# Kernel optimization log

Hardware: AMD Instinct MI355X
Metric: run time of the kernel (lower is better)

Reference implementation:

```python
import jax, jax.numpy as jnp
import numpy as np
from jax import lax

C1, C2 = 64, 128
B, H2, W2 = 16, 64, 64
EPS = 1e-5


def conv2d(x, w, b, pad):
    y = lax.conv_general_dilated(x, w, (1, 1), [(pad, pad), (pad, pad)],
                                 dimension_numbers=('NCHW', 'OIHW', 'NCHW'))
    return y + b[None, :, None, None]


def batchnorm(x, g, be):
    # training-mode BN (batch statistics), matching torch nn.BatchNorm2d default
    m = jnp.mean(x, axis=(0, 2, 3), keepdims=True)
    v = jnp.var(x, axis=(0, 2, 3), keepdims=True)
    return (x - m) * jax.lax.rsqrt(v + EPS) * g[None, :, None, None] + be[None, :, None, None]


def up2_bilinear_ac(x):
    # bilinear upsample x2 with align_corners=True (nn.UpsamplingBilinear2d)
    b, c, h, w = x.shape
    yy = jnp.arange(2 * h, dtype=x.dtype) * ((h - 1) / (2 * h - 1))
    xx = jnp.arange(2 * w, dtype=x.dtype) * ((w - 1) / (2 * w - 1))
    y0 = jnp.floor(yy).astype(jnp.int32); y1 = jnp.minimum(y0 + 1, h - 1)
    x0 = jnp.floor(xx).astype(jnp.int32); x1 = jnp.minimum(x0 + 1, w - 1)
    wy = (yy - y0.astype(x.dtype))
    wx = (xx - x0.astype(x.dtype))
    rows = x[:, :, y0, :] * (1 - wy)[:, None] + x[:, :, y1, :] * wy[:, None]
    return rows[:, :, :, x0] * (1 - wx) + rows[:, :, :, x1] * wx


def dilate(x, k):
    # grayscale morphological dilation with kxk ones kernel == sliding-window max
    return lax.reduce_window(x, -jnp.inf, lax.max, (1, 1, k, k), (1, 1, 1, 1), 'SAME')


def pixel_shuffle2(x):
    b, c, h, w = x.shape
    x = x.reshape(b, c // 4, 2, 2, h, w)
    return x.transpose(0, 1, 4, 2, 5, 3).reshape(b, c // 4, 2 * h, 2 * w)


def setup_inputs() -> dict:
    key = jax.random.key(0)
    ks = jax.random.split(key, 16)
    s = 0.05
    d = {
        'cur_x': jax.random.normal(ks[0], (B, C1, 2 * H2, 2 * W2), jnp.float32),
        'dep_x': jax.random.normal(ks[1], (B, C2, H2, W2), jnp.float32),
        'in_map': jax.random.normal(ks[2], (B, 1, H2, W2), jnp.float32),
        'up_w': jax.random.normal(ks[3], (4 * C1, C2, 3, 3), jnp.float32) * s,
        'up_b': jnp.zeros((4 * C1,), jnp.float32),
        'up_g': jnp.ones((4 * C1,), jnp.float32),
        'up_be': jnp.zeros((4 * C1,), jnp.float32),
        'conv2_w': jax.random.normal(ks[4], (C1, C1, 3, 3), jnp.float32) * s,
        'conv2_b': jnp.zeros((C1,), jnp.float32),
        'beta': jnp.ones((1,), jnp.float32),
        'd1_w': jax.random.normal(ks[5], (C1, C1, 3, 3), jnp.float32) * s,
        'd1_b': jnp.zeros((C1,), jnp.float32),
        'd1_g': jnp.ones((C1,), jnp.float32),
        'd1_be': jnp.zeros((C1,), jnp.float32),
        'd2_w': jax.random.normal(ks[6], (C1, C1, 3, 3), jnp.float32) * s,
        'd2_b': jnp.zeros((C1,), jnp.float32),
        'd2_g': jnp.ones((C1,), jnp.float32),
        'd2_be': jnp.zeros((C1,), jnp.float32),
        'd3_w': jax.random.normal(ks[7], (C1, C1, 3, 3), jnp.float32) * s,
        'd3_b': jnp.zeros((C1,), jnp.float32),
        'd3_g': jnp.ones((C1,), jnp.float32),
        'd3_be': jnp.zeros((C1,), jnp.float32),
        'out_w': jax.random.normal(ks[8], (1, C1, 7, 7), jnp.float32) * s,
        'out_b': jnp.zeros((1,), jnp.float32),
    }
    return d


def reference(cur_x, dep_x, in_map, up_w, up_b, up_g, up_be, conv2_w, conv2_b, beta,
              d1_w, d1_b, d1_g, d1_be, d2_w, d2_b, d2_g, d2_be, d3_w, d3_b, d3_g, d3_be,
              out_w, out_b):
    # up: conv(C2 -> 4*C1) + BN + ReLU, then PixelShuffle(2)
    dep = jax.nn.relu(batchnorm(conv2d(dep_x, up_w, up_b, 1), up_g, up_be))
    dep = pixel_shuffle2(dep)                       # [B, C1, H, W]
    imap = jax.nn.sigmoid(up2_bilinear_ac(in_map))  # [B, 1, H, W]
    # focus_background: dilated(map) - map (increase_input_map is identity, sf=1)
    increase_map = dilate(imap, 3) - imap
    b_feature = cur_x * increase_map
    fn = conv2d(b_feature, conv2_w, conv2_b, 1)
    r = jax.nn.relu(batchnorm(conv2d(dep + beta * fn, d1_w, d1_b, 1), d1_g, d1_be))
    r = jax.nn.relu(batchnorm(conv2d(r, d2_w, d2_b, 1), d2_g, d2_be))
    r = jax.nn.relu(batchnorm(conv2d(r, d3_w, d3_b, 1), d3_g, d3_be))
    output_map = conv2d(r, out_w, out_b, 3)
    return (r, output_map)
```

## Files before the change

kernel.cpp:

```cpp
#include <hip/hip_runtime.h>
#include <hip/hip_bf16.h>

using bf16 = __hip_bfloat16;
typedef __attribute__((ext_vector_type(8))) short bfrag;
typedef __attribute__((ext_vector_type(4))) float ffrag;

__device__ __forceinline__ float b2f(bf16 v) { return __bfloat162float(v); }
__device__ __forceinline__ float ldin(const void* p, int i, int isbf) {
    return isbf ? b2f(((const bf16*)p)[i]) : ((const float*)p)[i];
}
__device__ __forceinline__ void split2(float v, unsigned short& h, unsigned short& l) {
    bf16 hb = __float2bfloat16(v);
    h = __bfloat16_as_ushort(hb);
    l = __bfloat16_as_ushort(__float2bfloat16(v - __bfloat162float(hb)));
}

__global__ __launch_bounds__(256)
void prep_kernel(const unsigned* __restrict__ cur_x,
                 const void* __restrict__ up_w, const void* __restrict__ c2_w,
                 const void* __restrict__ d1_w, const void* __restrict__ d2_w,
                 const void* __restrict__ d3_w,
                 unsigned short* __restrict__ wbase,
                 float* __restrict__ accum, int* __restrict__ flagout)
{
    __shared__ int s_flag;
    const int tid = threadIdx.x;
    if (tid < 64) {
        int cnt = 0;
        for (int i = tid; i < 256; i += 64) {
            unsigned e = (cur_x[i] >> 7) & 0xFFu;
            cnt += (e >= 110u && e <= 135u) ? 1 : 0;
        }
#pragma unroll
        for (int off = 32; off > 0; off >>= 1) cnt += __shfl_down(cnt, off, 64);
        if (tid == 0) s_flag = (cnt >= 128) ? 1 : 0;
    }
    __syncthreads();
    const int isbf = s_flag;
    if (blockIdx.x == 0) {
        if (tid == 0) *flagout = isbf;
        for (int i = tid; i < 896; i += 256) accum[i] = 0.f;
    }
    int o = blockIdx.x * 256 + tid;
    if (o >= 442368) return;
    const void* w;
    int CIN, NCH, NCOG, lo;
    size_t hoff, losz;
    if (o < 294912) {
        w = up_w; CIN = 128; NCH = 4; NCOG = 16; hoff = 0; lo = o; losz = 294912;
    } else {
        int t = (o - 294912) / 36864;
        lo = (o - 294912) - t * 36864;
        CIN = 64; NCH = 2; NCOG = 4;
        hoff = 589824 + (size_t)t * 73728;
        losz = 36864;
        w = (t == 0) ? c2_w : (t == 1) ? d1_w : (t == 2) ? d2_w : d3_w;
    }
    int j = lo & 7;
    int l = (lo >> 3) & 63;
    int fb = lo >> 9;
    int cg = fb % NCOG;
    int t2 = fb / NCOG;
    int ch = t2 % NCH;
    int tap = t2 / NCH;
    int co = cg * 16 + (l & 15);
    int ci = ch * 32 + (l >> 4) * 8 + j;
    float v = ldin(w, (co * CIN + ci) * 9 + tap, isbf);
    unsigned short h, l2;
    split2(v, h, l2);
    wbase[hoff + lo] = h;
    wbase[hoff + losz + lo] = l2;
}

__global__ __launch_bounds__(256)
void dep_nhwc_kernel(const void* __restrict__ in, unsigned short* __restrict__ outp,
                     const int* __restrict__ flagp)
{
    __shared__ unsigned short s_h[64][65];
    __shared__ unsigned short s_l[64][65];
    const int isbf = *flagp;
    const int pb = blockIdx.x, cb = blockIdx.y, b = blockIdx.z;
    for (int i = threadIdx.x; i < 4096; i += 256) {
        int ci = i >> 6, pi = i & 63;
        float v = ldin(in, ((b * 128 + cb * 64 + ci) << 12) + (pb << 6) + pi, isbf);
        unsigned short h, l;
        split2(v, h, l);
        s_h[ci][pi] = h;
        if (!isbf) s_l[ci][pi] = l;
    }
    __syncthreads();
    for (int i = threadIdx.x; i < 4096; i += 256) {
        int ci = i & 63, pi = i >> 6;
        size_t o = ((size_t)(b * 4096 + pb * 64 + pi) << 7) + cb * 64 + ci;
        outp[o] = s_h[ci][pi];
        if (!isbf) outp[8388608 + o] = s_l[ci][pi];
    }
}

template<int CIN, int COUT, int H, int W, int ROWS, int WCO, int MODE,
         bool SMAP, bool EPI, bool BNIN, bool STATS, int MINW, int DTMODE = -1>
__global__ __launch_bounds__(256, MINW)
void conv3_mfma(const void* __restrict__ in,
                const unsigned short* __restrict__ whi,
                const unsigned short* __restrict__ wlo,
                const void* __restrict__ bias,
                const float* __restrict__ imapF,
                const float* __restrict__ dep,
                const void* __restrict__ betap,
                const float* __restrict__ accum,
                const void* __restrict__ bng, const void* __restrict__ bnbe,
                float* __restrict__ out, const int* __restrict__ flagp,
                float* __restrict__ sacc, int statC)
{
    constexpr int NCH  = CIN / 32;
    constexpr int NCOG = COUT / 16;
    constexpr int NCT  = W / 64;
    constexpr int W2h  = 66;
    constexpr int NP   = (ROWS + 2) * W2h;
    constexpr int NPs  = NP + 1;
    constexpr int NE   = 4 * NP;
    constexpr int NF   = (64 / WCO) / 16;
    constexpr int STCO = 64 / WCO;
    constexpr size_t PLANE = (size_t)16 * H * W * CIN;
    constexpr bool NOLO = (DTMODE == 1) && (MODE == 2) && !SMAP;

    if (DTMODE >= 0 && *flagp != DTMODE) return;
    const int isbf = (DTMODE >= 0) ? DTMODE : *flagp;

    __shared__ int4 s_hi[4 * NPs];
    __shared__ int4 s_lo[NOLO ? 1 : 4 * NPs];
    __shared__ float s_ss[BNIN ? 128 : 1];
    __shared__ float s_sm[SMAP ? NP : 1];
    float (*s_st)[4][STCO] = (float (*)[4][STCO])s_hi;

    const bool uselo = !(isbf && (MODE == 2 || (MODE == 1 && !SMAP)));
    const int tid  = threadIdx.x;
    const int r0   = (blockIdx.x / NCT) * ROWS;
    const int x0   = (blockIdx.x % NCT) * 64;
    const int bimg = r0 / H;
    const int y0im = bimg * H;
    const int coB  = blockIdx.y;

    if (BNIN) {
        if (tid < CIN) {
            const float n = (float)(16 * H * W);
            float S = accum[tid], S2 = accum[CIN + tid];
            float m = S / n;
            float var = fmaxf(S2 / n - m * m, 0.f);
            float scv = ldin(bng, tid, isbf) * rsqrtf(var + 1e-5f);
            s_ss[2 * tid]     = scv;
            s_ss[2 * tid + 1] = ldin(bnbe, tid, isbf) - m * scv;
        }
    }
    if (SMAP) {
        const float* ip = imapF + ((size_t)bimg << 14);
        for (int i = tid; i < NP; i += 256) {
            int rr = i / W2h, cc = i - rr * W2h;
            int gy = r0 - 1 + rr, gx = x0 - 1 + cc;
            float sm = 0.f;
            if (gy >= y0im && gy < y0im + H && (unsigned)gx < (unsigned)W) {
                int y = gy - y0im;
                float ctr = ip[(y << 7) + gx];
                float mx = ctr;
#pragma unroll
                for (int dy = -1; dy <= 1; dy++) {
                    int yy = y + dy;
                    if ((unsigned)yy < 128u) {
#pragma unroll
                        for (int dx = -1; dx <= 1; dx++) {
                            int xx = gx + dx;
                            if ((unsigned)xx < 128u) mx = fmaxf(mx, ip[(yy << 7) + xx]);
                        }
                    }
                }
                sm = mx - ctr;
            }
            s_sm[i] = sm;
        }
    }

    const int lane = tid & 63;
    const int wv = tid >> 6;
    const int wpx = wv / WCO, wco = wv % WCO;
    const int lx = lane & 15;
    const int gq = lane >> 4;

    ffrag acc[4][NF];
#pragma unroll
    for (int mf = 0; mf < 4; mf++)
#pragma unroll
        for (int nf = 0; nf < NF; nf++) acc[mf][nf] = ffrag{0.f, 0.f, 0.f, 0.f};

    for (int ch = 0; ch < NCH; ch++) {
        const int c0 = ch * 32;
        __syncthreads();
        for (int e = tid; e < NE; e += 256) {
            int gg, pixin;
            if (MODE == 1) { gg = e / NP; pixin = e - gg * NP; }
            else           { gg = e & 3;  pixin = e >> 2; }
            int rr = pixin / W2h;
            int cc2 = pixin - rr * W2h;
            int gy = r0 - 1 + rr;
            int gx = x0 - 1 + cc2;
            bool ok = (gy >= y0im) && (gy < y0im + H) && ((unsigned)gx < (unsigned)W);
            if (MODE == 2) {
                int4 hv = make_int4(0, 0, 0, 0), lv = make_int4(0, 0, 0, 0);
                if (ok) {
                    size_t eb = (size_t)(gy * W + gx) * CIN + c0 + 8 * gg;
                    hv = *(const int4*)((const unsigned short*)in + eb);
                    if (!isbf) lv = *(const int4*)((const unsigned short*)in + PLANE + eb);
                }
                s_hi[gg * NPs + pixin] = hv;
                if (!isbf && !NOLO) s_lo[gg * NPs + pixin] = lv;
            } else {
                float v[8];
                if (ok) {
                    if (MODE == 1) {
                        int y = gy - y0im;
                        float sm = SMAP ? s_sm[pixin] : 1.f;
#pragma unroll
                        for (int j = 0; j < 8; j++) {
                            int gi = ((bimg * CIN + c0 + 8 * gg + j) * H + y) * W + gx;
                            v[j] = ldin(in, gi, isbf) * sm;
                        }
                    } else {
                        const float* up = (const float*)in +
                            ((size_t)gy * W + gx) * CIN + c0 + 8 * gg;
                        float4 q0 = *(const float4*)up;
                        float4 q1 = *(const float4*)(up + 4);
                        v[0] = q0.x; v[1] = q0.y; v[2] = q0.z; v[3] = q0.w;
                        v[4] = q1.x; v[5] = q1.y; v[6] = q1.z; v[7] = q1.w;
                        if (BNIN) {
#pragma unroll
                            for (int j = 0; j < 8; j++) {
                                int chn = c0 + 8 * gg + j;
                                v[j] = fmaxf(fmaf(v[j], s_ss[2 * chn], s_ss[2 * chn + 1]), 0.f);
                            }
                        }
                    }
                } else {
#pragma unroll
                    for (int j = 0; j < 8; j++) v[j] = 0.f;
                }
                unsigned hp[4], lp[4];
#pragma unroll
                for (int j2 = 0; j2 < 4; j2++) {
                    bf16 h0b = __float2bfloat16(v[2 * j2]);
                    bf16 h1b = __float2bfloat16(v[2 * j2 + 1]);
                    hp[j2] = (unsigned)__bfloat16_as_ushort(h0b) |
                             ((unsigned)__bfloat16_as_ushort(h1b) << 16);
                    if (uselo) {
                        unsigned short l0 = __bfloat16_as_ushort(
                            __float2bfloat16(v[2 * j2] - b2f(h0b)));
                        unsigned short l1 = __bfloat16_as_ushort(
                            __float2bfloat16(v[2 * j2 + 1] - b2f(h1b)));
                        lp[j2] = (unsigned)l0 | ((unsigned)l1 << 16);
                    }
                }
                s_hi[gg * NPs + pixin] = make_int4(hp[0], hp[1], hp[2], hp[3]);
                if (uselo && !NOLO)
                    s_lo[gg * NPs + pixin] = make_int4(lp[0], lp[1], lp[2], lp[3]);
            }
        }
        __syncthreads();
#pragma unroll
        for (int tap = 0; tap < 9; tap++) {
            const int ky = tap / 3, kx = tap % 3;
            bfrag ah[4];
#pragma unroll
            for (int mf = 0; mf < 4; mf++) {
                int p = 64 * wpx + 16 * mf;
                int rI = (p >> 6) + ky;
                int cI = (p & 63) + kx + lx;
                int pix = rI * W2h + cI;
                ah[mf] = ((const bfrag*)s_hi)[gq * NPs + pix];
            }
            bfrag bh[NF];
#pragma unroll
            for (int nf = 0; nf < NF; nf++) {
                int fb = (tap * NCH + ch) * NCOG + coB * 4 + wco * NF + nf;
                bh[nf] = ((const bfrag*)(whi + (size_t)fb * 512))[lane];
            }
#pragma unroll
            for (int nf = 0; nf < NF; nf++)
#pragma unroll
                for (int mf = 0; mf < 4; mf++)
                    acc[mf][nf] = __builtin_amdgcn_mfma_f32_16x16x32_bf16(
                        ah[mf], bh[nf], acc[mf][nf], 0, 0, 0);
            if (!NOLO && uselo) {
                bfrag al[4];
#pragma unroll
                for (int mf = 0; mf < 4; mf++) {
                    int p = 64 * wpx + 16 * mf;
                    int rI = (p >> 6) + ky;
                    int cI = (p & 63) + kx + lx;
                    int pix = rI * W2h + cI;
                    al[mf] = ((const bfrag*)s_lo)[gq * NPs + pix];
                }
#pragma unroll
                for (int nf = 0; nf < NF; nf++)
#pragma unroll
                    for (int mf = 0; mf < 4; mf++)
                        acc[mf][nf] = __builtin_amdgcn_mfma_f32_16x16x32_bf16(
                            al[mf], bh[nf], acc[mf][nf], 0, 0, 0);
            }
            if (!isbf) {
                bfrag ah2[4];
#pragma unroll
                for (int mf = 0; mf < 4; mf++) {
                    int p = 64 * wpx + 16 * mf;
                    int rI = (p >> 6) + ky;
                    int cI = (p & 63) + kx + lx;
                    int pix = rI * W2h + cI;
                    ah2[mf] = ((const bfrag*)s_hi)[gq * NPs + pix];
                }
                bfrag bl[NF];
#pragma unroll
                for (int nf = 0; nf < NF; nf++) {
                    int fb = (tap * NCH + ch) * NCOG + coB * 4 + wco * NF + nf;
                    bl[nf] = ((const bfrag*)(wlo + (size_t)fb * 512))[lane];
                }
#pragma unroll
                for (int nf = 0; nf < NF; nf++)
#pragma unroll
                    for (int mf = 0; mf < 4; mf++)
                        acc[mf][nf] = __builtin_amdgcn_mfma_f32_16x16x32_bf16(
                            ah2[mf], bl[nf], acc[mf][nf], 0, 0, 0);
            }
        }
    }
    const float beta = EPI ? ldin(betap, 0, isbf) : 0.f;
    float sl[NF], s2l[NF];
#pragma unroll
    for (int nf = 0; nf < NF; nf++) { sl[nf] = 0.f; s2l[nf] = 0.f; }
#pragma unroll
    for (int nf = 0; nf < NF; nf++) {
        int co = coB * 64 + wco * STCO + nf * 16 + lx;
        float bi = ldin(bias, co, isbf);
#pragma unroll
        for (int mf = 0; mf < 4; mf++) {
#pragma unroll
            for (int r2 = 0; r2 < 4; r2++) {
                int p = 64 * wpx + 16 * mf + gq * 4 + r2;
                int grow = r0 + (p >> 6);
                int gcol = x0 + (p & 63);
                size_t oi = ((size_t)grow * W + gcol) * COUT + co;
                float vo = acc[mf][nf][r2] + bi;
                if (EPI) vo = dep[oi] + beta * vo;
                out[oi] = vo;
                if (STATS) {
                    sl[nf] += vo;
                    s2l[nf] = fmaf(vo, vo, s2l[nf]);
                }
            }
        }
    }
    if (STATS) {
        __syncthreads();
#pragma unroll
        for (int nf = 0; nf < NF; nf++) {
            float s = sl[nf], q = s2l[nf];
            s += __shfl_xor(s, 16, 64); s += __shfl_xor(s, 32, 64);
            q += __shfl_xor(q, 16, 64); q += __shfl_xor(q, 32, 64);
            if (gq == 0) {
                s_st[0][wv][nf * 16 + lx] = s;
                s_st[1][wv][nf * 16 + lx] = q;
            }
        }
        __syncthreads();
        if (tid < 128) {
            int which = tid >> 6, c = tid & 63;
            float v;
            if (WCO == 1) {
                v = s_st[which][0][c] + s_st[which][1][c] +
                    s_st[which][2][c] + s_st[which][3][c];
            } else {
                int wc = c >> 5, ci = c & 31;
                v = s_st[which][wc][ci] + s_st[which][2 + wc][ci];
            }
            atomicAdd(&sacc[which * statC + coB * 64 + c], v);
        }
    }
}

__global__ __launch_bounds__(256)
void shuffle_bn_nhwc_kernel(const float* __restrict__ u, const float* __restrict__ accum,
                            const void* __restrict__ g, const void* __restrict__ be,
                            float* __restrict__ dep, const int* __restrict__ flagp)
{
    int isbf = *flagp;
    int tid = threadIdx.x;
    int c = tid & 63, ps = tid >> 6;
    float sc[4], sh[4];
#pragma unroll
    for (int q = 0; q < 4; q++) {
        int chn = 4 * c + q;
        float S = accum[chn], S2 = accum[256 + chn];
        const float n = 65536.f;
        float m = S / n;
        float var = fmaxf(S2 / n - m * m, 0.f);
        sc[q] = ldin(g, chn, isbf) * rsqrtf(var + 1e-5f);
        sh[q] = ldin(be, chn, isbf) - m * sc[q];
    }
    for (int sp = blockIdx.x * 4 + ps; sp < 65536; sp += gridDim.x * 4) {
        float4 q4 = *(const float4*)(u + (size_t)sp * 256 + 4 * c);
        float vals[4] = {q4.x, q4.y, q4.z, q4.w};
        int b = sp >> 12, rem = sp & 4095, y2 = rem >> 6, x2 = rem & 63;
#pragma unroll
        for (int dy = 0; dy < 2; dy++)
#pragma unroll
            for (int dx = 0; dx < 2; dx++) {
                int q = 2 * dy + dx;
                float v = fmaxf(fmaf(vals[q], sc[q], sh[q]), 0.f);
                size_t op = (size_t)(b * 128 + 2 * y2 + dy) * 128 + (2 * x2 + dx);
                dep[op * 64 + c] = v;
            }
    }
}

__global__ __launch_bounds__(256)
void imap_kernel(const void* __restrict__ im, float* __restrict__ imap,
                 const int* __restrict__ flagp)
{
    int isbf = *flagp;
    int idx = blockIdx.x * 256 + threadIdx.x;
    int x = idx & 127, y = (idx >> 7) & 127, b = idx >> 14;
    const float s = (float)(63.0 / 127.0);
    float yy = y * s, xx = x * s;
    int y0 = (int)yy, x0 = (int)xx;
    float wy = yy - y0, wx = xx - x0;
    int y1 = min(y0 + 1, 63), x1 = min(x0 + 1, 63);
    int base = b << 12;
    float v00 = ldin(im, base + (y0 << 6) + x0, isbf);
    float v01 = ldin(im, base + (y0 << 6) + x1, isbf);
    float v10 = ldin(im, base + (y1 << 6) + x0, isbf);
    float v11 = ldin(im, base + (y1 << 6) + x1, isbf);
    float r0 = v00 * (1.f - wy) + v10 * wy;
    float r1 = v01 * (1.f - wy) + v11 * wy;
    float v = r0 * (1.f - wx) + r1 * wx;
    imap[idx] = 1.f / (1.f + expf(-v));
}

__global__ __launch_bounds__(256)
void bn_out_kernel(const float* __restrict__ u, const float* __restrict__ accum,
                   const void* __restrict__ g, const void* __restrict__ be,
                   float* __restrict__ r3, void* __restrict__ dout,
                   const int* __restrict__ flagp)
{
    int isbf = *flagp;
    int tid = threadIdx.x;
    int c = tid & 63, ps = tid >> 6;
    float S = accum[c], S2 = accum[64 + c];
    const float n = 262144.f;
    float m = S / n;
    float var = fmaxf(S2 / n - m * m, 0.f);
    float sc = ldin(g, c, isbf) * rsqrtf(var + 1e-5f);
    float sh = ldin(be, c, isbf) - m * sc;
    __shared__ float s[64][65];
    int pix0 = blockIdx.x * 64;
#pragma unroll
    for (int ii = 0; ii < 16; ii++) {
        int p = ps + 4 * ii;
        float v = u[(size_t)(pix0 + p) * 64 + c];
        s[p][c] = fmaxf(fmaf(v, sc, sh), 0.f);
    }
    __syncthreads();
    int x = c;
    int row = pix0 >> 7, col0 = pix0 & 127;
    int b = row >> 7, y = row & 127;
#pragma unroll
    for (int jj = 0; jj < 16; jj++) {
        int cc = ps + 4 * jj;
        float v = s[x][cc];
        size_t oi = (((size_t)(b * 64 + cc)) << 14) + (y << 7) + col0 + x;
        r3[oi] = v;
        if (isbf) ((bf16*)dout)[oi] = __float2bfloat16(v);
        else      ((float*)dout)[oi] = v;
    }
}

__global__ __launch_bounds__(256, 2)
void conv7x7_part_kernel(const float* __restrict__ r, const void* __restrict__ w,
                         float* __restrict__ outP, const int* __restrict__ flagp)
{
    __shared__ float s_in[4][70][22];
    __shared__ float s_w[16][49];
    const int isbf = *flagp;
    int tid = threadIdx.x;
    int tx = tid & 15, ty = tid >> 4;
    int x0 = blockIdx.x * 16, y0 = blockIdx.y * 64;
    int b = blockIdx.z >> 2, g = blockIdx.z & 3;
    for (int i = tid; i < 16 * 49; i += 256) {
        int ci = i / 49, k = i - ci * 49;
        s_w[ci][k] = ldin(w, (g * 16 + ci) * 49 + k, isbf);
    }
    float acc[4] = {0.f, 0.f, 0.f, 0.f};

    for (int c0 = 0; c0 < 16; c0 += 4) {
        __syncthreads();
        for (int i = tid; i < 4 * 70 * 22; i += 256) {
            int ci = i / (70 * 22);
            int rem = i - ci * (70 * 22);
            int rr = rem / 22, cc = rem - rr * 22;
            int gy = y0 + rr - 3, gx = x0 + cc - 3;
            float v = 0.f;
            if ((unsigned)gy < 128u && (unsigned)gx < 128u)
                v = r[((b * 64 + g * 16 + c0 + ci) << 14) + (gy << 7) + gx];
            s_in[ci][rr][cc] = v;
        }
        __syncthreads();
        for (int ci = 0; ci < 4; ci++) {
            float wr[49];
#pragma unroll
            for (int k = 0; k < 49; k++) wr[k] = s_w[c0 + ci][k];
#pragma unroll
            for (int rr = 0; rr < 10; rr++) {
                float row[7];
#pragma unroll
                for (int c = 0; c < 7; c++) row[c] = s_in[ci][4 * ty + rr][tx + c];
#pragma unroll
                for (int oy = 0; oy < 4; oy++) {
                    int ky = rr - oy;
                    if (ky >= 0 && ky <= 6) {
#pragma unroll
                        for (int kx = 0; kx < 7; kx++)
                            acc[oy] = fmaf(row[kx], wr[ky * 7 + kx], acc[oy]);
                    }
                }
            }
        }
    }
#pragma unroll
    for (int oy = 0; oy < 4; oy++) {
        int y = y0 + 4 * ty + oy;
        outP[(g << 18) + (b << 14) + (y << 7) + x0 + tx] = acc[oy];
    }
}

__global__ __launch_bounds__(256)
void finalize_out_kernel(const float* __restrict__ outP, const void* __restrict__ bias,
                         void* __restrict__ outv, const int* __restrict__ flagp)
{
    int isbf = *flagp;
    int i = blockIdx.x * 256 + threadIdx.x;
    float bi = ldin(bias, 0, isbf);
    float v = (outP[i] + outP[i + 262144]) +
              (outP[i + 2 * 262144] + outP[i + 3 * 262144]) + bi;
    int oidx = 16777216 + i;
    if (isbf) ((bf16*)outv)[oidx] = __float2bfloat16(v);
    else      ((float*)outv)[oidx] = v;
}

extern "C" void kernel_launch(void* const* d_in, const int* in_sizes, int n_in,
                              void* d_out, int out_size, void* d_ws, size_t ws_size,
                              hipStream_t stream)
{
    (void)in_sizes; (void)n_in; (void)out_size; (void)ws_size;

    const void* cur_x   = d_in[0];
    const void* dep_x   = d_in[1];
    const void* in_map  = d_in[2];
    const void* up_w    = d_in[3];
    const void* up_b    = d_in[4];
    const void* up_g    = d_in[5];
    const void* up_be   = d_in[6];
    const void* conv2_w = d_in[7];
    const void* conv2_b = d_in[8];
    const void* beta    = d_in[9];
    const void* d1_w = d_in[10];
    const void* d1_b = d_in[11];
    const void* d1_g = d_in[12];
    const void* d1_be = d_in[13];
    const void* d2_w = d_in[14];
    const void* d2_b = d_in[15];
    const void* d2_g = d_in[16];
    const void* d2_be = d_in[17];
    const void* d3_w = d_in[18];
    const void* d3_b = d_in[19];
    const void* d3_g = d_in[20];
    const void* d3_be = d_in[21];
    const void* out_w = d_in[22];
    const void* out_b = d_in[23];

    char* ws = (char*)d_ws;
    float* W0    = (float*)ws;
    float* W1    = (float*)(ws + 67108864);
    float* accum = (float*)(ws + 134217728);
    int*   flag  = (int*)(ws + 134221824);
    float* a0 = accum;
    float* a1 = accum + 512;
    float* a2 = accum + 640;
    float* a3 = accum + 768;

    char* sc = (char*)d_out;
    unsigned short* wbase = (unsigned short*)sc;
    unsigned short* whi1  = wbase;
    unsigned short* wlo1  = whi1 + 294912;
    unsigned short* whi2  = wlo1 + 294912;
    unsigned short* wlo2  = whi2 + 36864;
    unsigned short* whiD1 = wlo2 + 36864;
    unsigned short* wloD1 = whiD1 + 36864;
    unsigned short* whiD2 = wloD1 + 36864;
    unsigned short* wloD2 = whiD2 + 36864;
    unsigned short* whiD3 = wloD2 + 36864;
    unsigned short* wloD3 = whiD3 + 36864;
    float* imapF = (float*)(sc + 1769472);

    prep_kernel<<<1728, 256, 0, stream>>>((const unsigned*)cur_x,
        up_w, conv2_w, d1_w, d2_w, d3_w, wbase, accum, flag);
    dep_nhwc_kernel<<<dim3(64, 2, 16), 256, 0, stream>>>(
        dep_x, (unsigned short*)W1, flag);

    conv3_mfma<128, 256, 64, 64, 4, 1, 2, false, false, false, true, 6, 1>
        <<<dim3(256, 4), 256, 0, stream>>>((const void*)W1, whi1, wlo1, up_b,
            nullptr, nullptr, nullptr, nullptr, nullptr, nullptr, W0, flag, a0, 256);
    conv3_mfma<128, 256, 64, 64, 4, 1, 2, false, false, false, true, 3, 0>
        <<<dim3(256, 4), 256, 0, stream>>>((const void*)W1, whi1, wlo1, up_b,
            nullptr, nullptr, nullptr, nullptr, nullptr, nullptr, W0, flag, a0, 256);
    imap_kernel<<<1024, 256, 0, stream>>>(in_map, imapF, flag);
    shuffle_bn_nhwc_kernel<<<2048, 256, 0, stream>>>(W0, a0, up_g, up_be, W1, flag);
    conv3_mfma<64, 64, 128, 128, 2, 2, 1, true, true, false, false, 4>
        <<<dim3(2048, 1), 256, 0, stream>>>(cur_x, whi2, wlo2, conv2_b,
            imapF, W1, beta, nullptr, nullptr, nullptr, W0, flag, nullptr, 0);
    conv3_mfma<64, 64, 128, 128, 2, 2, 0, false, false, false, true, 4>
        <<<dim3(2048, 1), 256, 0, stream>>>(W0, whiD1, wloD1, d1_b,
            nullptr, nullptr, nullptr, nullptr, nullptr, nullptr, W1, flag, a1, 64);
    conv3_mfma<64, 64, 128, 128, 2, 2, 0, false, false, true, true, 4>
        <<<dim3(2048, 1), 256, 0, stream>>>(W1, whiD2, wloD2, d2_b,
            nullptr, nullptr, nullptr, a1, d1_g, d1_be, W0, flag, a2, 64);
    conv3_mfma<64, 64, 128, 128, 2, 2, 0, false, false, true, true, 4>
        <<<dim3(2048, 1), 256, 0, stream>>>(W0, whiD3, wloD3, d3_b,
            nullptr, nullptr, nullptr, a2, d2_g, d2_be, W1, flag, a3, 64);
    bn_out_kernel<<<4096, 256, 0, stream>>>(W1, a3, d3_g, d3_be, W0, d_out, flag);
    conv7x7_part_kernel<<<dim3(8, 2, 64), 256, 0, stream>>>(W0, out_w, W1, flag);
    finalize_out_kernel<<<1024, 256, 0, stream>>>(W1, out_b, d_out, flag);
}
```

Measured before the change: 786.4 us.

## Merge prep kernels, retile up-conv, swizzle blocks, reuse A fragments, skip redundant r3 write

Merges the weight prep, dep_x NHWC transpose and imap upsample kernels into one launch to cut launch overhead. The up-conv tile changes from 4 rows x 1 co-wave to 2 rows x 2 co-waves with a doubled grid and a different occupancy hint. A block-index swizzle is added to all conv launches to change the order tiles are scheduled in. The A-fragment reload for the low-weight MFMA pass is reused, the staging loop is unrolled, and the fp32 path skips writing a duplicate r3 copy by having the 7x7 conv read the output buffer directly. The swizzle assumes gridDim.x is divisible by 8, and the changed tiling may alter register pressure and occupancy.

```diff
diff --git a/kernel.cpp b/kernel.cpp
--- a/kernel.cpp
+++ b/kernel.cpp
@@ -16,13 +16,18 @@
 }
 
 __global__ __launch_bounds__(256)
-void prep_kernel(const unsigned* __restrict__ cur_x,
-                 const void* __restrict__ up_w, const void* __restrict__ c2_w,
-                 const void* __restrict__ d1_w, const void* __restrict__ d2_w,
-                 const void* __restrict__ d3_w,
-                 unsigned short* __restrict__ wbase,
-                 float* __restrict__ accum, int* __restrict__ flagout)
+void prep_all_kernel(const unsigned* __restrict__ cur_x,
+                     const void* __restrict__ up_w, const void* __restrict__ c2_w,
+                     const void* __restrict__ d1_w, const void* __restrict__ d2_w,
+                     const void* __restrict__ d3_w,
+                     const void* __restrict__ dep_x, const void* __restrict__ in_map,
+                     unsigned short* __restrict__ wbase,
+                     unsigned short* __restrict__ depout,
+                     float* __restrict__ imapF,
+                     float* __restrict__ accum, int* __restrict__ flagout)
 {
+    __shared__ unsigned short s_h[64][65];
+    __shared__ unsigned short s_l[64][65];
     __shared__ int s_flag;
     const int tid = threadIdx.x;
     if (tid < 64) {
@@ -37,68 +42,82 @@
     }
     __syncthreads();
     const int isbf = s_flag;
-    if (blockIdx.x == 0) {
+    const int bid = blockIdx.x;
+    if (bid == 0) {
         if (tid == 0) *flagout = isbf;
         for (int i = tid; i < 896; i += 256) accum[i] = 0.f;
     }
-    int o = blockIdx.x * 256 + tid;
-    if (o >= 442368) return;
-    const void* w;
-    int CIN, NCH, NCOG, lo;
-    size_t hoff, losz;
-    if (o < 294912) {
-        w = up_w; CIN = 128; NCH = 4; NCOG = 16; hoff = 0; lo = o; losz = 294912;
+    if (bid < 1728) {
+        int o = bid * 256 + tid;
+        if (o >= 442368) return;
+        const void* w;
+        int CIN, NCH, NCOG, lo;
+        size_t hoff, losz;
+        if (o < 294912) {
+            w = up_w; CIN = 128; NCH = 4; NCOG = 16; hoff = 0; lo = o; losz = 294912;
+        } else {
+            int t = (o - 294912) / 36864;
+            lo = (o - 294912) - t * 36864;
+            CIN = 64; NCH = 2; NCOG = 4;
+            hoff = 589824 + (size_t)t * 73728;
+            losz = 36864;
+            w = (t == 0) ? c2_w : (t == 1) ? d1_w : (t == 2) ? d2_w : d3_w;
+        }
+        int j = lo & 7;
+        int l = (lo >> 3) & 63;
+        int fb = lo >> 9;
+        int cg = fb % NCOG;
+        int t2 = fb / NCOG;
+        int ch = t2 % NCH;
+        int tap = t2 / NCH;
+        int co = cg * 16 + (l & 15);
+        int ci = ch * 32 + (l >> 4) * 8 + j;
+        float v = ldin(w, (co * CIN + ci) * 9 + tap, isbf);
+        unsigned short h, l2;
+        split2(v, h, l2);
+        wbase[hoff + lo] = h;
+        wbase[hoff + losz + lo] = l2;
+    } else if (bid < 3776) {
+        int lid = bid - 1728;
+        int pb = lid & 63, cb = (lid >> 6) & 1, b = lid >> 7;
+        for (int i = tid; i < 4096; i += 256) {
+            int ci = i >> 6, pi = i & 63;
+            float v = ldin(dep_x, ((b * 128 + cb * 64 + ci) << 12) + (pb << 6) + pi, isbf);
+            unsigned short h, l;
+            split2(v, h, l);
+            s_h[ci][pi] = h;
+            if (!isbf) s_l[ci][pi] = l;
+        }
+        __syncthreads();
+        for (int i = tid; i < 4096; i += 256) {
+            int ci = i & 63, pi = i >> 6;
+            size_t o = ((size_t)(b * 4096 + pb * 64 + pi) << 7) + cb * 64 + ci;
+            depout[o] = s_h[ci][pi];
+            if (!isbf) depout[8388608 + o] = s_l[ci][pi];
+        }
     } else {
-        int t = (o - 294912) / 36864;
-        lo = (o - 294912) - t * 36864;
-        CIN = 64; NCH = 2; NCOG = 4;
-        hoff = 589824 + (size_t)t * 73728;
-        losz = 36864;
-        w = (t == 0) ? c2_w : (t == 1) ? d1_w : (t == 2) ? d2_w : d3_w;
-    }
-    int j = lo & 7;
-    int l = (lo >> 3) & 63;
-    int fb = lo >> 9;
-    int cg = fb % NCOG;
-    int t2 = fb / NCOG;
-    int ch = t2 % NCH;
-    int tap = t2 / NCH;
-    int co = cg * 16 + (l & 15);
-    int ci = ch * 32 + (l >> 4) * 8 + j;
-    float v = ldin(w, (co * CIN + ci) * 9 + tap, isbf);
-    unsigned short h, l2;
-    split2(v, h, l2);
-    wbase[hoff + lo] = h;
-    wbase[hoff + losz + lo] = l2;
-}
-
-__global__ __launch_bounds__(256)
-void dep_nhwc_kernel(const void* __restrict__ in, unsigned short* __restrict__ outp,
-                     const int* __restrict__ flagp)
-{
-    __shared__ unsigned short s_h[64][65];
-    __shared__ unsigned short s_l[64][65];
-    const int isbf = *flagp;
-    const int pb = blockIdx.x, cb = blockIdx.y, b = blockIdx.z;
-    for (int i = threadIdx.x; i < 4096; i += 256) {
-        int ci = i >> 6, pi = i & 63;
-        float v = ldin(in, ((b * 128 + cb * 64 + ci) << 12) + (pb << 6) + pi, isbf);
-        unsigned short h, l;
-        split2(v, h, l);
-        s_h[ci][pi] = h;
-        if (!isbf) s_l[ci][pi] = l;
-    }
-    __syncthreads();
-    for (int i = threadIdx.x; i < 4096; i += 256) {
-        int ci = i & 63, pi = i >> 6;
-        size_t o = ((size_t)(b * 4096 + pb * 64 + pi) << 7) + cb * 64 + ci;
-        outp[o] = s_h[ci][pi];
-        if (!isbf) outp[8388608 + o] = s_l[ci][pi];
+        int idx = (bid - 3776) * 256 + tid;
+        int x = idx & 127, y = (idx >> 7) & 127, b = idx >> 14;
+        const float s = (float)(63.0 / 127.0);
+        float yy = y * s, xx = x * s;
+        int y0 = (int)yy, x0 = (int)xx;
+        float wy = yy - y0, wx = xx - x0;
+        int y1 = min(y0 + 1, 63), x1 = min(x0 + 1, 63);
+        int base = b << 12;
+        float v00 = ldin(in_map, base + (y0 << 6) + x0, isbf);
+        float v01 = ldin(in_map, base + (y0 << 6) + x1, isbf);
+        float v10 = ldin(in_map, base + (y1 << 6) + x0, isbf);
+        float v11 = ldin(in_map, base + (y1 << 6) + x1, isbf);
+        float r0 = v00 * (1.f - wy) + v10 * wy;
+        float r1 = v01 * (1.f - wy) + v11 * wy;
+        float v = r0 * (1.f - wx) + r1 * wx;
+        imapF[idx] = 1.f / (1.f + expf(-v));
     }
 }
 
 template<int CIN, int COUT, int H, int W, int ROWS, int WCO, int MODE,
-         bool SMAP, bool EPI, bool BNIN, bool STATS, int MINW, int DTMODE = -1>
+         bool SMAP, bool EPI, bool BNIN, bool STATS, int MINW,
+         int DTMODE = -1, bool SWZ = false>
 __global__ __launch_bounds__(256, MINW)
 void conv3_mfma(const void* __restrict__ in,
                 const unsigned short* __restrict__ whi,
@@ -119,6 +138,7 @@
     constexpr int NP   = (ROWS + 2) * W2h;
     constexpr int NPs  = NP + 1;
     constexpr int NE   = 4 * NP;
+    constexpr int NIT  = (NE + 255) / 256;
     constexpr int NF   = (64 / WCO) / 16;
     constexpr int STCO = 64 / WCO;
     constexpr size_t PLANE = (size_t)16 * H * W * CIN;
@@ -135,8 +155,10 @@
 
     const bool uselo = !(isbf && (MODE == 2 || (MODE == 1 && !SMAP)));
     const int tid  = threadIdx.x;
-    const int r0   = (blockIdx.x / NCT) * ROWS;
-    const int x0   = (blockIdx.x % NCT) * 64;
+    int bidx = blockIdx.x;
+    if (SWZ) bidx = ((bidx & 7) * (gridDim.x >> 3)) + (bidx >> 3);
+    const int r0   = (bidx / NCT) * ROWS;
+    const int x0   = (bidx % NCT) * 64;
     const int bimg = r0 / H;
     const int y0im = bimg * H;
     const int coB  = blockIdx.y;
@@ -194,7 +216,10 @@
     for (int ch = 0; ch < NCH; ch++) {
         const int c0 = ch * 32;
         __syncthreads();
-        for (int e = tid; e < NE; e += 256) {
+#pragma unroll
+        for (int it = 0; it < NIT; it++) {
+            int e = tid + it * 256;
+            if (e >= NE) break;
             int gg, pixin;
             if (MODE == 1) { gg = e / NP; pixin = e - gg * NP; }
             else           { gg = e & 3;  pixin = e >> 2; }
@@ -270,9 +295,7 @@
 #pragma unroll
             for (int mf = 0; mf < 4; mf++) {
                 int p = 64 * wpx + 16 * mf;
-                int rI = (p >> 6) + ky;
-                int cI = (p & 63) + kx + lx;
-                int pix = rI * W2h + cI;
+                int pix = ((p >> 6) + ky) * W2h + (p & 63) + kx + lx;
                 ah[mf] = ((const bfrag*)s_hi)[gq * NPs + pix];
             }
             bfrag bh[NF];
@@ -292,9 +315,7 @@
 #pragma unroll
                 for (int mf = 0; mf < 4; mf++) {
                     int p = 64 * wpx + 16 * mf;
-                    int rI = (p >> 6) + ky;
-                    int cI = (p & 63) + kx + lx;
-                    int pix = rI * W2h + cI;
+                    int pix = ((p >> 6) + ky) * W2h + (p & 63) + kx + lx;
                     al[mf] = ((const bfrag*)s_lo)[gq * NPs + pix];
                 }
 #pragma unroll
@@ -305,15 +326,6 @@
                             al[mf], bh[nf], acc[mf][nf], 0, 0, 0);
             }
             if (!isbf) {
-                bfrag ah2[4];
-#pragma unroll
-                for (int mf = 0; mf < 4; mf++) {
-                    int p = 64 * wpx + 16 * mf;
-                    int rI = (p >> 6) + ky;
-                    int cI = (p & 63) + kx + lx;
-                    int pix = rI * W2h + cI;
-                    ah2[mf] = ((const bfrag*)s_hi)[gq * NPs + pix];
-                }
                 bfrag bl[NF];
 #pragma unroll
                 for (int nf = 0; nf < NF; nf++) {
@@ -325,7 +337,7 @@
 #pragma unroll
                     for (int mf = 0; mf < 4; mf++)
                         acc[mf][nf] = __builtin_amdgcn_mfma_f32_16x16x32_bf16(
-                            ah2[mf], bl[nf], acc[mf][nf], 0, 0, 0);
+                            ah[mf], bl[nf], acc[mf][nf], 0, 0, 0);
             }
         }
     }
@@ -416,29 +428,6 @@
                 dep[op * 64 + c] = v;
             }
     }
-}
-
-__global__ __launch_bounds__(256)
-void imap_kernel(const void* __restrict__ im, float* __restrict__ imap,
-                 const int* __restrict__ flagp)
-{
-    int isbf = *flagp;
-    int idx = blockIdx.x * 256 + threadIdx.x;
-    int x = idx & 127, y = (idx >> 7) & 127, b = idx >> 14;
-    const float s = (float)(63.0 / 127.0);
-    float yy = y * s, xx = x * s;
-    int y0 = (int)yy, x0 = (int)xx;
-    float wy = yy - y0, wx = xx - x0;
-    int y1 = min(y0 + 1, 63), x1 = min(x0 + 1, 63);
-    int base = b << 12;
-    float v00 = ldin(im, base + (y0 << 6) + x0, isbf);
-    float v01 = ldin(im, base + (y0 << 6) + x1, isbf);
-    float v10 = ldin(im, base + (y1 << 6) + x0, isbf);
-    float v11 = ldin(im, base + (y1 << 6) + x1, isbf);
-    float r0 = v00 * (1.f - wy) + v10 * wy;
-    float r1 = v01 * (1.f - wy) + v11 * wy;
-    float v = r0 * (1.f - wx) + r1 * wx;
-    imap[idx] = 1.f / (1.f + expf(-v));
 }
 
 __global__ __launch_bounds__(256)
@@ -473,19 +462,24 @@
         int cc = ps + 4 * jj;
         float v = s[x][cc];
         size_t oi = (((size_t)(b * 64 + cc)) << 14) + (y << 7) + col0 + x;
-        r3[oi] = v;
-        if (isbf) ((bf16*)dout)[oi] = __float2bfloat16(v);
-        else      ((float*)dout)[oi] = v;
+        if (isbf) {
+            r3[oi] = v;
+            ((bf16*)dout)[oi] = __float2bfloat16(v);
+        } else {
+            ((float*)dout)[oi] = v;
+        }
     }
 }
 
 __global__ __launch_bounds__(256, 2)
-void conv7x7_part_kernel(const float* __restrict__ r, const void* __restrict__ w,
+void conv7x7_part_kernel(const float* __restrict__ r3ws, const void* __restrict__ dout,
+                         const void* __restrict__ w,
                          float* __restrict__ outP, const int* __restrict__ flagp)
 {
     __shared__ float s_in[4][70][22];
     __shared__ float s_w[16][49];
     const int isbf = *flagp;
+    const float* r = isbf ? r3ws : (const float*)dout;
     int tid = threadIdx.x;
     int tx = tid & 15, ty = tid >> 4;
     int x0 = blockIdx.x * 16, y0 = blockIdx.y * 64;
@@ -606,32 +600,30 @@
     unsigned short* wloD3 = whiD3 + 36864;
     float* imapF = (float*)(sc + 1769472);
 
-    prep_kernel<<<1728, 256, 0, stream>>>((const unsigned*)cur_x,
-        up_w, conv2_w, d1_w, d2_w, d3_w, wbase, accum, flag);
-    dep_nhwc_kernel<<<dim3(64, 2, 16), 256, 0, stream>>>(
-        dep_x, (unsigned short*)W1, flag);
-
-    conv3_mfma<128, 256, 64, 64, 4, 1, 2, false, false, false, true, 6, 1>
-        <<<dim3(256, 4), 256, 0, stream>>>((const void*)W1, whi1, wlo1, up_b,
+    prep_all_kernel<<<4800, 256, 0, stream>>>((const unsigned*)cur_x,
+        up_w, conv2_w, d1_w, d2_w, d3_w, dep_x, in_map,
+        wbase, (unsigned short*)W1, imapF, accum, flag);
+
+    conv3_mfma<128, 256, 64, 64, 2, 2, 2, false, false, false, true, 6, 1, true>
+        <<<dim3(512, 4), 256, 0, stream>>>((const void*)W1, whi1, wlo1, up_b,
             nullptr, nullptr, nullptr, nullptr, nullptr, nullptr, W0, flag, a0, 256);
-    conv3_mfma<128, 256, 64, 64, 4, 1, 2, false, false, false, true, 3, 0>
-        <<<dim3(256, 4), 256, 0, stream>>>((const void*)W1, whi1, wlo1, up_b,
+    conv3_mfma<128, 256, 64, 64, 2, 2, 2, false, false, false, true, 4, 0, true>
+        <<<dim3(512, 4), 256, 0, stream>>>((const void*)W1, whi1, wlo1, up_b,
             nullptr, nullptr, nullptr, nullptr, nullptr, nullptr, W0, flag, a0, 256);
-    imap_kernel<<<1024, 256, 0, stream>>>(in_map, imapF, flag);
     shuffle_bn_nhwc_kernel<<<2048, 256, 0, stream>>>(W0, a0, up_g, up_be, W1, flag);
-    conv3_mfma<64, 64, 128, 128, 2, 2, 1, true, true, false, false, 4>
+    conv3_mfma<64, 64, 128, 128, 2, 2, 1, true, true, false, false, 4, -1, true>
         <<<dim3(2048, 1), 256, 0, stream>>>(cur_x, whi2, wlo2, conv2_b,
             imapF, W1, beta, nullptr, nullptr, nullptr, W0, flag, nullptr, 0);
-    conv3_mfma<64, 64, 128, 128, 2, 2, 0, false, false, false, true, 4>
+    conv3_mfma<64, 64, 128, 128, 2, 2, 0, false, false, false, true, 4, -1, true>
         <<<dim3(2048, 1), 256, 0, stream>>>(W0, whiD1, wloD1, d1_b,
             nullptr, nullptr, nullptr, nullptr, nullptr, nullptr, W1, flag, a1, 64);
-    conv3_mfma<64, 64, 128, 128, 2, 2, 0, false, false, true, true, 4>
+    conv3_mfma<64, 64, 128, 128, 2, 2, 0, false, false, true, true, 4, -1, true>
         <<<dim3(2048, 1), 256, 0, stream>>>(W1, whiD2, wloD2, d2_b,
             nullptr, nullptr, nullptr, a1, d1_g, d1_be, W0, flag, a2, 64);
-    conv3_mfma<64, 64, 128, 128, 2, 2, 0, false, false, true, true, 4>
+    conv3_mfma<64, 64, 128, 128, 2, 2, 0, false, false, true, true, 4, -1, true>
         <<<dim3(2048, 1), 256, 0, stream>>>(W0, whiD3, wloD3, d3_b,
             nullptr, nullptr, nullptr, a2, d2_g, d2_be, W1, flag, a3, 64);
     bn_out_kernel<<<4096, 256, 0, stream>>>(W1, a3, d3_g, d3_be, W0, d_out, flag);
-    conv7x7_part_kernel<<<dim3(8, 2, 64), 256, 0, stream>>>(W0, out_w, W1, flag);
+    conv7x7_part_kernel<<<dim3(8, 2, 64), 256, 0, stream>>>(W0, d_out, out_w, W1, flag);
     finalize_out_kernel<<<1024, 256, 0, stream>>>(W1, out_b, d_out, flag);
 }
```

New measurement: 765.3 us. 2.7% less time.
